# Kernel optimization log

Measured on AMD Instinct MI355X. Metric: run time of the kernel, lower is better.

Reference implementation:

```python
import jax, jax.numpy as jnp
import numpy as np
from jax import lax

K = 35
PAD = K // 2  # 17

def _maxpool_same(x):
    # x: [B, H, W]; torch MaxPool2d pads with -inf, stride 1, same spatial size
    return lax.reduce_window(
        x, -jnp.inf, lax.max,
        window_dimensions=(1, K, K),
        window_strides=(1, 1, 1),
        padding=[(0, 0), (PAD, PAD), (PAD, PAD)],
    )

def setup_inputs() -> dict:
    key = jax.random.key(0)
    k1, k2 = jax.random.split(key)
    shape = (16, 3, 512, 512)
    restored = jax.random.uniform(k1, shape, dtype=jnp.float32)
    target = jax.random.uniform(k2, shape, dtype=jnp.float32)
    return {"restored": restored, "target": target}

def reference(restored, target):
    r = _maxpool_same(jnp.min(restored, axis=1))  # channel-min then 35x35 max
    t = _maxpool_same(jnp.min(target, axis=1))
    out = jnp.mean(jnp.abs(r - t))
    return jax.nn.sigmoid(out)
```

## Files before the change

kernel.cpp:

```cpp
#include <hip/hip_runtime.h>
#include <math.h>

#define WID 512
#define HEI 512
#define NB  16
#define HW  ((size_t)HEI * WID)
#define NEG_INF (-INFINITY)

typedef float f4 __attribute__((ext_vector_type(4)));

__device__ __forceinline__ float qmax4(f4 v) {
    return fmaxf(fmaxf(v.x, v.y), fmaxf(v.z, v.w));
}

__device__ __forceinline__ f4 hwin35(const f4* __restrict__ rp, int c4) {
    f4 vv[11];
    #pragma unroll
    for (int i = 0; i < 11; ++i) vv[i] = rp[c4 + i];
    float q[10];
    #pragma unroll
    for (int i = 1; i <= 9; ++i) q[i] = qmax4(vv[i]);
    float Q28 = fmaxf(fmaxf(fmaxf(q[2], q[3]), fmaxf(q[4], q[5])),
                      fmaxf(fmaxf(q[6], q[7]), q[8]));
    float Q18 = fmaxf(Q28, q[1]);
    float Q29 = fmaxf(Q28, q[9]);
    float s01 = fmaxf(vv[9].x, vv[9].y);
    float s23 = fmaxf(vv[1].z, vv[1].w);
    f4 o;
    o.x = fmaxf(fmaxf(Q18, vv[0].w), s01);
    o.y = fmaxf(Q18, fmaxf(s01, vv[9].z));
    o.z = fmaxf(fmaxf(Q29, vv[1].y), s23);
    o.w = fmaxf(Q29, fmaxf(s23, vv[10].x));
    return o;
}

__global__ __launch_bounds__(256) void hmax_kernel(
    const float* __restrict__ rin, const float* __restrict__ tin,
    float* __restrict__ ws)
{
    __shared__ float sm[4][552];
    const int tid = threadIdx.x;
    const int wv  = tid >> 6;
    const int l   = tid & 63;
    const int h   = blockIdx.x * 4 + wv;
    const int z   = blockIdx.y;
    const int b   = z & 15;
    const float* __restrict__ in = (z < NB) ? rin : tin;
    const float* __restrict__ p  = in + (size_t)b * 3 * HW + (size_t)h * WID;

    if (tid < 160) {
        int r = tid / 40, j = tid % 40;
        sm[r][(j < 20) ? j : (j + 512)] = NEG_INF;
    }

    const f4* __restrict__ p0 = (const f4*)p;
    const f4* __restrict__ p1 = (const f4*)(p + HW);
    const f4* __restrict__ p2 = (const f4*)(p + 2 * HW);
    f4 a0 = __builtin_nontemporal_load(p0 + l);
    f4 b0 = __builtin_nontemporal_load(p1 + l);
    f4 c0 = __builtin_nontemporal_load(p2 + l);
    f4 a1 = __builtin_nontemporal_load(p0 + l + 64);
    f4 b1 = __builtin_nontemporal_load(p1 + l + 64);
    f4 c1 = __builtin_nontemporal_load(p2 + l + 64);
    f4 v0, v1;
    v0.x = fminf(fminf(a0.x, b0.x), c0.x);
    v0.y = fminf(fminf(a0.y, b0.y), c0.y);
    v0.z = fminf(fminf(a0.z, b0.z), c0.z);
    v0.w = fminf(fminf(a0.w, b0.w), c0.w);
    v1.x = fminf(fminf(a1.x, b1.x), c1.x);
    v1.y = fminf(fminf(a1.y, b1.y), c1.y);
    v1.z = fminf(fminf(a1.z, b1.z), c1.z);
    v1.w = fminf(fminf(a1.w, b1.w), c1.w);
    *(f4*)&sm[wv][20 + 4 * l]        = v0;
    *(f4*)&sm[wv][20 + 4 * (l + 64)] = v1;
    __syncthreads();

    const f4* __restrict__ smr = (const f4*)sm[wv];
    f4 o0 = hwin35(smr, l);
    f4 o1 = hwin35(smr, l + 64);
    f4* __restrict__ wp = (f4*)(ws + (size_t)z * HW + (size_t)h * WID);
    wp[l]      = o0;
    wp[l + 64] = o1;
}

__global__ __launch_bounds__(256, 3) void vmax_kernel(
    const float* __restrict__ ws, float* __restrict__ acc,
    float* __restrict__ out)
{
    __shared__ float cm2[162][64];
    __shared__ float red[4];
    const int tid = threadIdx.x;
    const int col = tid & 63;
    const int ty  = tid >> 6;
    const int w0  = blockIdx.x * 64;
    const int h0  = blockIdx.y * 128;
    const int b   = blockIdx.z;

    float rtv[32];
    float tsum = 0.0f;

    #pragma unroll
    for (int tensor = 0; tensor < 2; ++tensor) {
        const float* __restrict__ pb = ws + (size_t)(tensor * NB + b) * HW;

        for (int i = tid; i < 2592; i += 256) {
            int r = i >> 4, c4 = i & 15;
            int hh = h0 - 17 + r;
            f4 v = {NEG_INF, NEG_INF, NEG_INF, NEG_INF};
            if (hh >= 0 && hh < HEI)
                v = ((const f4*)pb)[hh * 128 + (w0 >> 2) + c4];
            *(f4*)&cm2[r][4 * c4] = v;
        }
        __syncthreads();

        #pragma unroll
        for (int g = 0; g < 2; ++g) {
            const int base = ty * 32 + g * 16;
            float vc[50];
            #pragma unroll
            for (int i = 0; i < 50; ++i) vc[i] = cm2[base + i][col];
            float q[12];
            #pragma unroll
            for (int i = 0; i < 12; ++i)
                q[i] = fmaxf(fmaxf(vc[4*i], vc[4*i+1]),
                             fmaxf(vc[4*i+2], vc[4*i+3]));
            #pragma unroll
            for (int m = 0; m < 4; ++m) {
                float Qc = fmaxf(fmaxf(fmaxf(q[m+1], q[m+2]), fmaxf(q[m+3], q[m+4])),
                                 fmaxf(fmaxf(q[m+5], q[m+6]), q[m+7]));
                float A  = fmaxf(Qc, q[m+8]);
                float o0 = fmaxf(fmaxf(Qc, q[m]),
                                 fmaxf(fmaxf(vc[4*m+32], vc[4*m+33]), vc[4*m+34]));
                float o1 = fmaxf(A, fmaxf(fmaxf(vc[4*m+1], vc[4*m+2]), vc[4*m+3]));
                float o2 = fmaxf(A, fmaxf(fmaxf(vc[4*m+2], vc[4*m+3]), vc[4*m+36]));
                float o3 = fmaxf(A, fmaxf(fmaxf(vc[4*m+3], vc[4*m+36]), vc[4*m+37]));
                const int k = g * 16 + 4 * m;
                if (tensor == 0) {
                    rtv[k] = o0; rtv[k+1] = o1; rtv[k+2] = o2; rtv[k+3] = o3;
                } else {
                    tsum += fabsf(rtv[k]   - o0) + fabsf(rtv[k+1] - o1)
                          + fabsf(rtv[k+2] - o2) + fabsf(rtv[k+3] - o3);
                }
            }
        }
        __syncthreads();
    }

    #pragma unroll
    for (int off = 32; off > 0; off >>= 1)
        tsum += __shfl_down(tsum, off, 64);
    if (col == 0) red[ty] = tsum;
    __syncthreads();
    if (tid == 0) {
        float bs = red[0] + red[1] + red[2] + red[3];
        atomicAdd(acc, bs);
        __threadfence();
        unsigned tk = atomicAdd((unsigned*)(acc + 1), 1u);
        if (tk == 511u) {
            float s = atomicAdd(acc, 0.0f);
            out[0] = 1.0f / (1.0f + expf(-s / 4194304.0f));
        }
    }
}

extern "C" void kernel_launch(void* const* d_in, const int* in_sizes, int n_in,
                              void* d_out, int out_size, void* d_ws, size_t ws_size,
                              hipStream_t stream) {
    const float* rin = (const float*)d_in[0];
    const float* tin = (const float*)d_in[1];
    float* out = (float*)d_out;

    float* wsf = (float*)d_ws;
    float* acc = wsf + (size_t)2 * NB * HW;

    hipMemsetAsync(acc, 0, 2 * sizeof(float), stream);

    dim3 gA(HEI / 4, 2 * NB);
    hipLaunchKernelGGL(hmax_kernel, gA, dim3(256), 0, stream, rin, tin, wsf);

    dim3 gB(WID / 64, HEI / 128, NB);
    hipLaunchKernelGGL(vmax_kernel, gB, dim3(256), 0, stream, wsf, acc, out);
}
```

Before: 144.3 us.

## Fuse horizontal and vertical max passes into one cooperative kernel with grid sync

Replaces the memset plus two kernel launches with a single cooperative launch of 512 blocks. Each block first computes the channel-min and horizontal 35-wide max for 32 rows, using double-buffered register prefetch of the next row group. A grid-wide sync follows, then the same block does the vertical max and abs-diff reduction. This removes launch and memset overhead and overlaps loads with compute, at the cost of far fewer blocks in the first phase, a grid barrier, and shared memory enlarged to the vertical-phase size, which may lower occupancy.

```diff
diff --git a/kernel.cpp b/kernel.cpp
--- a/kernel.cpp
+++ b/kernel.cpp
@@ -1,4 +1,5 @@
 #include <hip/hip_runtime.h>
+#include <hip/hip_cooperative_groups.h>
 #include <math.h>
 
 #define WID 512
@@ -8,9 +9,21 @@
 #define NEG_INF (-INFINITY)
 
 typedef float f4 __attribute__((ext_vector_type(4)));
+namespace cg = cooperative_groups;
+
+#define NTL(p) __builtin_nontemporal_load(p)
 
 __device__ __forceinline__ float qmax4(f4 v) {
     return fmaxf(fmaxf(v.x, v.y), fmaxf(v.z, v.w));
+}
+
+__device__ __forceinline__ f4 min3v(f4 a, f4 b, f4 c) {
+    f4 v;
+    v.x = fminf(fminf(a.x, b.x), c.x);
+    v.y = fminf(fminf(a.y, b.y), c.y);
+    v.z = fminf(fminf(a.z, b.z), c.z);
+    v.w = fminf(fminf(a.w, b.w), c.w);
+    return v;
 }
 
 __device__ __forceinline__ f4 hwin35(const f4* __restrict__ rp, int c4) {
@@ -34,131 +47,148 @@
     return o;
 }
 
-__global__ __launch_bounds__(256) void hmax_kernel(
+__global__ __launch_bounds__(256) void ccp_coop_kernel(
     const float* __restrict__ rin, const float* __restrict__ tin,
-    float* __restrict__ ws)
+    float* __restrict__ ws, float* __restrict__ acc, float* __restrict__ out)
 {
-    __shared__ float sm[4][552];
+    __shared__ float smem[162 * 64 + 4];
     const int tid = threadIdx.x;
     const int wv  = tid >> 6;
     const int l   = tid & 63;
-    const int h   = blockIdx.x * 4 + wv;
-    const int z   = blockIdx.y;
-    const int b   = z & 15;
-    const float* __restrict__ in = (z < NB) ? rin : tin;
-    const float* __restrict__ p  = in + (size_t)b * 3 * HW + (size_t)h * WID;
-
-    if (tid < 160) {
-        int r = tid / 40, j = tid % 40;
-        sm[r][(j < 20) ? j : (j + 512)] = NEG_INF;
+    const int bx  = blockIdx.x;
+
+    if (bx == 0 && tid < 2) acc[tid] = 0.0f;
+
+    {
+        float (*sm)[4][552] = (float (*)[4][552])smem;
+        const int z = bx >> 4;
+        const int b = z & 15;
+        const float* __restrict__ in = (z < NB) ? rin : tin;
+        const float* __restrict__ pc = in + (size_t)b * 3 * HW;
+        const int hbase = (bx & 15) * 32;
+
+        if (tid < 160) {
+            int r = tid / 40, j = tid % 40;
+            int jj = (j < 20) ? j : (j + 512);
+            sm[0][r][jj] = NEG_INF;
+            sm[1][r][jj] = NEG_INF;
+        }
+
+        f4 ld[2][6];
+        {
+            const float* pr = pc + (size_t)(hbase + wv) * WID;
+            ld[0][0] = NTL((const f4*)pr + l);
+            ld[0][1] = NTL((const f4*)(pr + HW) + l);
+            ld[0][2] = NTL((const f4*)(pr + 2 * HW) + l);
+            ld[0][3] = NTL((const f4*)pr + l + 64);
+            ld[0][4] = NTL((const f4*)(pr + HW) + l + 64);
+            ld[0][5] = NTL((const f4*)(pr + 2 * HW) + l + 64);
+        }
+        #pragma unroll
+        for (int t = 0; t < 8; ++t) {
+            const int cur = t & 1, nxt = cur ^ 1;
+            if (t < 7) {
+                const float* pr = pc + (size_t)(hbase + 4 * (t + 1) + wv) * WID;
+                ld[nxt][0] = NTL((const f4*)pr + l);
+                ld[nxt][1] = NTL((const f4*)(pr + HW) + l);
+                ld[nxt][2] = NTL((const f4*)(pr + 2 * HW) + l);
+                ld[nxt][3] = NTL((const f4*)pr + l + 64);
+                ld[nxt][4] = NTL((const f4*)(pr + HW) + l + 64);
+                ld[nxt][5] = NTL((const f4*)(pr + 2 * HW) + l + 64);
+            }
+            f4 v0 = min3v(ld[cur][0], ld[cur][1], ld[cur][2]);
+            f4 v1 = min3v(ld[cur][3], ld[cur][4], ld[cur][5]);
+            float (*S)[552] = sm[cur];
+            *(f4*)&S[wv][20 + 4 * l]        = v0;
+            *(f4*)&S[wv][20 + 4 * (l + 64)] = v1;
+            __syncthreads();
+            const f4* smr = (const f4*)S[wv];
+            f4 o0 = hwin35(smr, l);
+            f4 o1 = hwin35(smr, l + 64);
+            const int h = hbase + 4 * t + wv;
+            f4* wp = (f4*)(ws + (size_t)z * HW + (size_t)h * WID);
+            wp[l]      = o0;
+            wp[l + 64] = o1;
+        }
     }
 
-    const f4* __restrict__ p0 = (const f4*)p;
-    const f4* __restrict__ p1 = (const f4*)(p + HW);
-    const f4* __restrict__ p2 = (const f4*)(p + 2 * HW);
-    f4 a0 = __builtin_nontemporal_load(p0 + l);
-    f4 b0 = __builtin_nontemporal_load(p1 + l);
-    f4 c0 = __builtin_nontemporal_load(p2 + l);
-    f4 a1 = __builtin_nontemporal_load(p0 + l + 64);
-    f4 b1 = __builtin_nontemporal_load(p1 + l + 64);
-    f4 c1 = __builtin_nontemporal_load(p2 + l + 64);
-    f4 v0, v1;
-    v0.x = fminf(fminf(a0.x, b0.x), c0.x);
-    v0.y = fminf(fminf(a0.y, b0.y), c0.y);
-    v0.z = fminf(fminf(a0.z, b0.z), c0.z);
-    v0.w = fminf(fminf(a0.w, b0.w), c0.w);
-    v1.x = fminf(fminf(a1.x, b1.x), c1.x);
-    v1.y = fminf(fminf(a1.y, b1.y), c1.y);
-    v1.z = fminf(fminf(a1.z, b1.z), c1.z);
-    v1.w = fminf(fminf(a1.w, b1.w), c1.w);
-    *(f4*)&sm[wv][20 + 4 * l]        = v0;
-    *(f4*)&sm[wv][20 + 4 * (l + 64)] = v1;
-    __syncthreads();
-
-    const f4* __restrict__ smr = (const f4*)sm[wv];
-    f4 o0 = hwin35(smr, l);
-    f4 o1 = hwin35(smr, l + 64);
-    f4* __restrict__ wp = (f4*)(ws + (size_t)z * HW + (size_t)h * WID);
-    wp[l]      = o0;
-    wp[l + 64] = o1;
-}
-
-__global__ __launch_bounds__(256, 3) void vmax_kernel(
-    const float* __restrict__ ws, float* __restrict__ acc,
-    float* __restrict__ out)
-{
-    __shared__ float cm2[162][64];
-    __shared__ float red[4];
-    const int tid = threadIdx.x;
-    const int col = tid & 63;
-    const int ty  = tid >> 6;
-    const int w0  = blockIdx.x * 64;
-    const int h0  = blockIdx.y * 128;
-    const int b   = blockIdx.z;
-
-    float rtv[32];
-    float tsum = 0.0f;
-
-    #pragma unroll
-    for (int tensor = 0; tensor < 2; ++tensor) {
-        const float* __restrict__ pb = ws + (size_t)(tensor * NB + b) * HW;
-
-        for (int i = tid; i < 2592; i += 256) {
-            int r = i >> 4, c4 = i & 15;
-            int hh = h0 - 17 + r;
-            f4 v = {NEG_INF, NEG_INF, NEG_INF, NEG_INF};
-            if (hh >= 0 && hh < HEI)
-                v = ((const f4*)pb)[hh * 128 + (w0 >> 2) + c4];
-            *(f4*)&cm2[r][4 * c4] = v;
-        }
+    __threadfence();
+    cg::this_grid().sync();
+
+    {
+        float (*cm)[64] = (float (*)[64])smem;
+        float* red = smem + 162 * 64;
+        const int col = l;
+        const int ty  = wv;
+        const int w0  = (bx & 7) * 64;
+        const int h0  = ((bx >> 3) & 3) * 128;
+        const int b   = bx >> 5;
+
+        float rtv[32];
+        float tsum = 0.0f;
+
+        #pragma unroll
+        for (int tensor = 0; tensor < 2; ++tensor) {
+            const float* __restrict__ pb = ws + (size_t)(tensor * NB + b) * HW;
+
+            for (int i = tid; i < 2592; i += 256) {
+                int r = i >> 4, c4 = i & 15;
+                int hh = h0 - 17 + r;
+                f4 v = {NEG_INF, NEG_INF, NEG_INF, NEG_INF};
+                if (hh >= 0 && hh < HEI)
+                    v = ((const f4*)pb)[hh * 128 + (w0 >> 2) + c4];
+                *(f4*)&cm[r][4 * c4] = v;
+            }
+            __syncthreads();
+
+            #pragma unroll
+            for (int g = 0; g < 2; ++g) {
+                const int base = ty * 32 + g * 16;
+                float vc[50];
+                #pragma unroll
+                for (int i = 0; i < 50; ++i) vc[i] = cm[base + i][col];
+                float q[12];
+                #pragma unroll
+                for (int i = 0; i < 12; ++i)
+                    q[i] = fmaxf(fmaxf(vc[4*i], vc[4*i+1]),
+                                 fmaxf(vc[4*i+2], vc[4*i+3]));
+                #pragma unroll
+                for (int m = 0; m < 4; ++m) {
+                    float Qc = fmaxf(fmaxf(fmaxf(q[m+1], q[m+2]),
+                                           fmaxf(q[m+3], q[m+4])),
+                                     fmaxf(fmaxf(q[m+5], q[m+6]), q[m+7]));
+                    float A  = fmaxf(Qc, q[m+8]);
+                    float o0 = fmaxf(fmaxf(Qc, q[m]),
+                                     fmaxf(fmaxf(vc[4*m+32], vc[4*m+33]), vc[4*m+34]));
+                    float o1 = fmaxf(A, fmaxf(fmaxf(vc[4*m+1], vc[4*m+2]), vc[4*m+3]));
+                    float o2 = fmaxf(A, fmaxf(fmaxf(vc[4*m+2], vc[4*m+3]), vc[4*m+36]));
+                    float o3 = fmaxf(A, fmaxf(fmaxf(vc[4*m+3], vc[4*m+36]), vc[4*m+37]));
+                    const int k = g * 16 + 4 * m;
+                    if (tensor == 0) {
+                        rtv[k] = o0; rtv[k+1] = o1; rtv[k+2] = o2; rtv[k+3] = o3;
+                    } else {
+                        tsum += fabsf(rtv[k]   - o0) + fabsf(rtv[k+1] - o1)
+                              + fabsf(rtv[k+2] - o2) + fabsf(rtv[k+3] - o3);
+                    }
+                }
+            }
+            __syncthreads();
+        }
+
+        #pragma unroll
+        for (int off = 32; off > 0; off >>= 1)
+            tsum += __shfl_down(tsum, off, 64);
+        if (col == 0) red[ty] = tsum;
         __syncthreads();
-
-        #pragma unroll
-        for (int g = 0; g < 2; ++g) {
-            const int base = ty * 32 + g * 16;
-            float vc[50];
-            #pragma unroll
-            for (int i = 0; i < 50; ++i) vc[i] = cm2[base + i][col];
-            float q[12];
-            #pragma unroll
-            for (int i = 0; i < 12; ++i)
-                q[i] = fmaxf(fmaxf(vc[4*i], vc[4*i+1]),
-                             fmaxf(vc[4*i+2], vc[4*i+3]));
-            #pragma unroll
-            for (int m = 0; m < 4; ++m) {
-                float Qc = fmaxf(fmaxf(fmaxf(q[m+1], q[m+2]), fmaxf(q[m+3], q[m+4])),
-                                 fmaxf(fmaxf(q[m+5], q[m+6]), q[m+7]));
-                float A  = fmaxf(Qc, q[m+8]);
-                float o0 = fmaxf(fmaxf(Qc, q[m]),
-                                 fmaxf(fmaxf(vc[4*m+32], vc[4*m+33]), vc[4*m+34]));
-                float o1 = fmaxf(A, fmaxf(fmaxf(vc[4*m+1], vc[4*m+2]), vc[4*m+3]));
-                float o2 = fmaxf(A, fmaxf(fmaxf(vc[4*m+2], vc[4*m+3]), vc[4*m+36]));
-                float o3 = fmaxf(A, fmaxf(fmaxf(vc[4*m+3], vc[4*m+36]), vc[4*m+37]));
-                const int k = g * 16 + 4 * m;
-                if (tensor == 0) {
-                    rtv[k] = o0; rtv[k+1] = o1; rtv[k+2] = o2; rtv[k+3] = o3;
-                } else {
-                    tsum += fabsf(rtv[k]   - o0) + fabsf(rtv[k+1] - o1)
-                          + fabsf(rtv[k+2] - o2) + fabsf(rtv[k+3] - o3);
-                }
-            }
-        }
-        __syncthreads();
-    }
-
-    #pragma unroll
-    for (int off = 32; off > 0; off >>= 1)
-        tsum += __shfl_down(tsum, off, 64);
-    if (col == 0) red[ty] = tsum;
-    __syncthreads();
-    if (tid == 0) {
-        float bs = red[0] + red[1] + red[2] + red[3];
-        atomicAdd(acc, bs);
-        __threadfence();
-        unsigned tk = atomicAdd((unsigned*)(acc + 1), 1u);
-        if (tk == 511u) {
-            float s = atomicAdd(acc, 0.0f);
-            out[0] = 1.0f / (1.0f + expf(-s / 4194304.0f));
+        if (tid == 0) {
+            float bs = red[0] + red[1] + red[2] + red[3];
+            atomicAdd(acc, bs);
+            __threadfence();
+            unsigned tk = atomicAdd((unsigned*)(acc + 1), 1u);
+            if (tk == 511u) {
+                float s = atomicAdd(acc, 0.0f);
+                out[0] = 1.0f / (1.0f + expf(-s / 4194304.0f));
+            }
         }
     }
 }
@@ -173,11 +203,12 @@
     float* wsf = (float*)d_ws;
     float* acc = wsf + (size_t)2 * NB * HW;
 
-    hipMemsetAsync(acc, 0, 2 * sizeof(float), stream);
-
-    dim3 gA(HEI / 4, 2 * NB);
-    hipLaunchKernelGGL(hmax_kernel, gA, dim3(256), 0, stream, rin, tin, wsf);
-
-    dim3 gB(WID / 64, HEI / 128, NB);
-    hipLaunchKernelGGL(vmax_kernel, gB, dim3(256), 0, stream, wsf, acc, out);
-}
+    void* args[5];
+    args[0] = (void*)&rin;
+    args[1] = (void*)&tin;
+    args[2] = (void*)&wsf;
+    args[3] = (void*)&acc;
+    args[4] = (void*)&out;
+    hipLaunchCooperativeKernel((void*)ccp_coop_kernel, dim3(512), dim3(256),
+                               args, 0, stream);
+}
```

New measurement: 280.9 us. 94.6% more time.

## Load vertical-pass columns into registers directly and fold accumulator reset into hmax

Applied to the files above, without the earlier changes.

The vertical max kernel no longer stages a tile in shared memory. Each thread now loads a 66-row strip of one column straight into registers, with 32 output rows per thread and 256 columns per block, so there are no LDS writes, reads or barriers. In exchange each tile reads about twice as many halo rows from the workspace, and relies on L2 and the last-level cache to absorb them. The accumulator reset moves from a separate hipMemsetAsync into the first block of hmax_kernel, which removes one extra operation from the stream.

```diff
diff --git a/kernel.cpp b/kernel.cpp
--- a/kernel.cpp
+++ b/kernel.cpp
@@ -8,6 +8,8 @@
 #define NEG_INF (-INFINITY)
 
 typedef float f4 __attribute__((ext_vector_type(4)));
+
+#define NTL(p) __builtin_nontemporal_load(p)
 
 __device__ __forceinline__ float qmax4(f4 v) {
     return fmaxf(fmaxf(v.x, v.y), fmaxf(v.z, v.w));
@@ -36,7 +38,7 @@
 
 __global__ __launch_bounds__(256) void hmax_kernel(
     const float* __restrict__ rin, const float* __restrict__ tin,
-    float* __restrict__ ws)
+    float* __restrict__ ws, float* __restrict__ acc)
 {
     __shared__ float sm[4][552];
     const int tid = threadIdx.x;
@@ -48,6 +50,8 @@
     const float* __restrict__ in = (z < NB) ? rin : tin;
     const float* __restrict__ p  = in + (size_t)b * 3 * HW + (size_t)h * WID;
 
+    if (blockIdx.x == 0 && blockIdx.y == 0 && tid < 2) acc[tid] = 0.0f;
+
     if (tid < 160) {
         int r = tid / 40, j = tid % 40;
         sm[r][(j < 20) ? j : (j + 512)] = NEG_INF;
@@ -56,12 +60,12 @@
     const f4* __restrict__ p0 = (const f4*)p;
     const f4* __restrict__ p1 = (const f4*)(p + HW);
     const f4* __restrict__ p2 = (const f4*)(p + 2 * HW);
-    f4 a0 = __builtin_nontemporal_load(p0 + l);
-    f4 b0 = __builtin_nontemporal_load(p1 + l);
-    f4 c0 = __builtin_nontemporal_load(p2 + l);
-    f4 a1 = __builtin_nontemporal_load(p0 + l + 64);
-    f4 b1 = __builtin_nontemporal_load(p1 + l + 64);
-    f4 c1 = __builtin_nontemporal_load(p2 + l + 64);
+    f4 a0 = NTL(p0 + l);
+    f4 b0 = NTL(p1 + l);
+    f4 c0 = NTL(p2 + l);
+    f4 a1 = NTL(p0 + l + 64);
+    f4 b1 = NTL(p1 + l + 64);
+    f4 c1 = NTL(p2 + l + 64);
     f4 v0, v1;
     v0.x = fminf(fminf(a0.x, b0.x), c0.x);
     v0.y = fminf(fminf(a0.y, b0.y), c0.y);
@@ -83,57 +87,53 @@
     wp[l + 64] = o1;
 }
 
-__global__ __launch_bounds__(256, 3) void vmax_kernel(
+__global__ __launch_bounds__(256) void vmax_kernel(
     const float* __restrict__ ws, float* __restrict__ acc,
     float* __restrict__ out)
 {
-    __shared__ float cm2[162][64];
     __shared__ float red[4];
     const int tid = threadIdx.x;
-    const int col = tid & 63;
-    const int ty  = tid >> 6;
-    const int w0  = blockIdx.x * 64;
-    const int h0  = blockIdx.y * 128;
+    const int col = blockIdx.x * 256 + tid;
+    const int h0  = blockIdx.y * 32;
     const int b   = blockIdx.z;
 
     float rtv[32];
     float tsum = 0.0f;
 
-    #pragma unroll
+    #pragma unroll 1
     for (int tensor = 0; tensor < 2; ++tensor) {
         const float* __restrict__ pb = ws + (size_t)(tensor * NB + b) * HW;
 
-        for (int i = tid; i < 2592; i += 256) {
-            int r = i >> 4, c4 = i & 15;
-            int hh = h0 - 17 + r;
-            f4 v = {NEG_INF, NEG_INF, NEG_INF, NEG_INF};
-            if (hh >= 0 && hh < HEI)
-                v = ((const f4*)pb)[hh * 128 + (w0 >> 2) + c4];
-            *(f4*)&cm2[r][4 * c4] = v;
+        float v[66];
+        #pragma unroll
+        for (int i = 0; i < 66; ++i) {
+            int hh = h0 - 17 + i;
+            v[i] = (hh >= 0 && hh < HEI) ? pb[(size_t)hh * WID + col]
+                                         : NEG_INF;
         }
-        __syncthreads();
 
         #pragma unroll
         for (int g = 0; g < 2; ++g) {
-            const int base = ty * 32 + g * 16;
-            float vc[50];
-            #pragma unroll
-            for (int i = 0; i < 50; ++i) vc[i] = cm2[base + i][col];
             float q[12];
             #pragma unroll
             for (int i = 0; i < 12; ++i)
-                q[i] = fmaxf(fmaxf(vc[4*i], vc[4*i+1]),
-                             fmaxf(vc[4*i+2], vc[4*i+3]));
+                q[i] = fmaxf(fmaxf(v[g*16 + 4*i],     v[g*16 + 4*i + 1]),
+                             fmaxf(v[g*16 + 4*i + 2], v[g*16 + 4*i + 3]));
             #pragma unroll
             for (int m = 0; m < 4; ++m) {
-                float Qc = fmaxf(fmaxf(fmaxf(q[m+1], q[m+2]), fmaxf(q[m+3], q[m+4])),
+                float Qc = fmaxf(fmaxf(fmaxf(q[m+1], q[m+2]),
+                                       fmaxf(q[m+3], q[m+4])),
                                  fmaxf(fmaxf(q[m+5], q[m+6]), q[m+7]));
                 float A  = fmaxf(Qc, q[m+8]);
                 float o0 = fmaxf(fmaxf(Qc, q[m]),
-                                 fmaxf(fmaxf(vc[4*m+32], vc[4*m+33]), vc[4*m+34]));
-                float o1 = fmaxf(A, fmaxf(fmaxf(vc[4*m+1], vc[4*m+2]), vc[4*m+3]));
-                float o2 = fmaxf(A, fmaxf(fmaxf(vc[4*m+2], vc[4*m+3]), vc[4*m+36]));
-                float o3 = fmaxf(A, fmaxf(fmaxf(vc[4*m+3], vc[4*m+36]), vc[4*m+37]));
+                                 fmaxf(fmaxf(v[g*16+4*m+32], v[g*16+4*m+33]),
+                                       v[g*16+4*m+34]));
+                float o1 = fmaxf(A, fmaxf(fmaxf(v[g*16+4*m+1], v[g*16+4*m+2]),
+                                          v[g*16+4*m+3]));
+                float o2 = fmaxf(A, fmaxf(fmaxf(v[g*16+4*m+2], v[g*16+4*m+3]),
+                                          v[g*16+4*m+36]));
+                float o3 = fmaxf(A, fmaxf(fmaxf(v[g*16+4*m+3], v[g*16+4*m+36]),
+                                          v[g*16+4*m+37]));
                 const int k = g * 16 + 4 * m;
                 if (tensor == 0) {
                     rtv[k] = o0; rtv[k+1] = o1; rtv[k+2] = o2; rtv[k+3] = o3;
@@ -143,13 +143,14 @@
                 }
             }
         }
-        __syncthreads();
     }
 
+    const int lane = tid & 63;
+    const int wv   = tid >> 6;
     #pragma unroll
     for (int off = 32; off > 0; off >>= 1)
         tsum += __shfl_down(tsum, off, 64);
-    if (col == 0) red[ty] = tsum;
+    if (lane == 0) red[wv] = tsum;
     __syncthreads();
     if (tid == 0) {
         float bs = red[0] + red[1] + red[2] + red[3];
@@ -173,11 +174,9 @@
     float* wsf = (float*)d_ws;
     float* acc = wsf + (size_t)2 * NB * HW;
 
-    hipMemsetAsync(acc, 0, 2 * sizeof(float), stream);
+    dim3 gA(HEI / 4, 2 * NB);
+    hipLaunchKernelGGL(hmax_kernel, gA, dim3(256), 0, stream, rin, tin, wsf, acc);
 
-    dim3 gA(HEI / 4, 2 * NB);
-    hipLaunchKernelGGL(hmax_kernel, gA, dim3(256), 0, stream, rin, tin, wsf);
-
-    dim3 gB(WID / 64, HEI / 128, NB);
+    dim3 gB(2, 16, NB);
     hipLaunchKernelGGL(vmax_kernel, gB, dim3(256), 0, stream, wsf, acc, out);
 }
```

Result: no change. 145.4 us (+0.7%).
